# Kernel tuning notes

Measured on AMD Instinct MI355X. Metric: run time of the kernel, lower is better.

The kernel has to match this reference:

```python
import jax, jax.numpy as jnp
import numpy as np


def setup_inputs() -> dict:
    key = jax.random.key(0)
    ks = jax.random.split(key, 4)
    B, S, D, E = 8, 4096, 2048, 64
    scale = 1.0 / np.sqrt(D)
    return {
        "x": jax.random.normal(ks[0], (B, S, D), dtype=jnp.float32),
        "W_route": jax.random.normal(ks[1], (E, D), dtype=jnp.float32) * scale,
        "b_route": jnp.zeros((E,), dtype=jnp.float32),
        "W_noise": jax.random.normal(ks[2], (E, D), dtype=jnp.float32) * scale,
        "b_noise": jnp.zeros((E,), dtype=jnp.float32),
        "noise_eps": jax.random.normal(ks[3], (B, S, E), dtype=jnp.float32),
    }


TOP_K = 2


def reference(x, W_route, b_route, W_noise, b_noise, noise_eps):
    # Dual linear projections: [B,S,D] @ [D,E] -> [B,S,E]
    logits = jnp.einsum("bsd,ed->bse", x, W_route) + b_route
    noise_logits = jnp.einsum("bsd,ed->bse", x, W_noise) + b_noise
    noisy_logits = logits + noise_eps * jax.nn.softplus(noise_logits)

    B, S, E = noisy_logits.shape
    flat = noisy_logits.reshape(B * S, E)
    top_vals, top_idx = jax.lax.top_k(flat, TOP_K)  # [N,K]

    # Scatter top-k values into -inf background, then softmax over experts.
    neg_inf = jnp.full_like(flat, -jnp.inf)
    rows = jnp.arange(B * S)[:, None]
    sparse = neg_inf.at[rows, top_idx].set(top_vals)
    router_output = jax.nn.softmax(sparse, axis=-1).reshape(B, S, E)
    indices = top_idx.reshape(B, S, TOP_K)
    return router_output, indices
```

## Files before the change

kernel.cpp:

```cpp
#include <hip/hip_runtime.h>
#include <math.h>

typedef _Float16 f16;
typedef __attribute__((ext_vector_type(8))) _Float16 half8;
typedef __attribute__((ext_vector_type(4))) float f32x4;

#define NEXP 64
#define TM 64
#define L_STRIDE 132

__device__ __forceinline__ float softplus_f(float x) {
    return fmaxf(x, 0.0f) + log1pf(expf(-fabsf(x)));
}

__device__ __forceinline__ void lds_dma16(const void* g, void* l) {
    __builtin_amdgcn_global_load_lds(
        (const __attribute__((address_space(1))) unsigned int*)g,
        (__attribute__((address_space(3))) unsigned int*)l, 16, 0, 0);
}

__device__ __forceinline__ void cvt_split(const float4 a, const float4 b,
                                          half8& hv, half8& lv) {
    const float vv[8] = {a.x, a.y, a.z, a.w, b.x, b.y, b.z, b.w};
#pragma unroll
    for (int j = 0; j < 8; ++j) {
        const f16 h = (f16)vv[j];
        hv[j] = h;
        lv[j] = (f16)((vv[j] - (float)h) * 4096.0f);
    }
}

__global__ void wsplit_kernel(const float* __restrict__ Wr,
                              const float* __restrict__ Wn,
                              f16* __restrict__ ws, int D) {
    const int per_col = D >> 3;
    const int t = blockIdx.x * blockDim.x + threadIdx.x;
    const int col = t / per_col;
    const int k0  = (t - col * per_col) * 8;
    if (col >= 128) return;
    const float* src = (col < NEXP) ? &Wr[(size_t)col * D] : &Wn[(size_t)(col - NEXP) * D];
    const float4 v0 = *(const float4*)&src[k0];
    const float4 v1 = *(const float4*)&src[k0 + 4];
    half8 hi, lo;
    cvt_split(v0, v1, hi, lo);
    const int kc = k0 >> 5, q = (k0 >> 3) & 3;
    const size_t base = (size_t)kc * 8192 + (size_t)q * 1024 + (size_t)col * 8;
    *(half8*)&ws[base]        = hi;
    *(half8*)&ws[base + 4096] = lo;
}

__global__ __launch_bounds__(256, 3)
void router_mfma_kernel(const float* __restrict__ x,
                        const f16* __restrict__ wsW,
                        const float* __restrict__ br,
                        const float* __restrict__ bn,
                        const float* __restrict__ eps,
                        float* __restrict__ out,
                        int N, int D) {
    __shared__ union alignas(16) {
        struct { f16 B[2][8192]; f16 A[2][4096]; } st;
        float L[TM][L_STRIDE];
    } sm;
    __shared__ float biasLDS[128];
    __shared__ float p1s[TM], p2s[TM];
    __shared__ int   i1s[TM], i2s[TM];

    const int tid  = threadIdx.x;
    const int lane = tid & 63;
    const int w    = tid >> 6;
    const int rowbase = blockIdx.x * TM;
    const int wr = w & 1, wc = w >> 1;
    const int quad = lane >> 4;
    const int l16  = lane & 15;

    if (tid < 128) biasLDS[tid] = (tid < NEXP) ? br[tid] : bn[tid - NEXP];

    f32x4 accM[2][4], accC[2][4];
#pragma unroll
    for (int i = 0; i < 2; ++i)
#pragma unroll
        for (int j = 0; j < 4; ++j) {
            accM[i][j] = (f32x4){0.f, 0.f, 0.f, 0.f};
            accC[i][j] = (f32x4){0.f, 0.f, 0.f, 0.f};
        }

    const int sr = tid >> 2;
    const int sq = tid & 3;
    const float* xrow = &x[(size_t)(rowbase + sr) * D + sq * 8];
    const int nkc = D >> 5;

    {
        const char* gsrc = (const char*)wsW + (size_t)0 * 16384 + w * 4096 + lane * 16;
        char* ldst = (char*)&sm.st.B[0][0] + w * 4096;
#pragma unroll
        for (int i = 0; i < 4; ++i) lds_dma16(gsrc + i * 1024, ldst + i * 1024);
        const float4 a0 = *(const float4*)&xrow[0];
        const float4 a1 = *(const float4*)&xrow[4];
        half8 hv, lv;
        cvt_split(a0, a1, hv, lv);
        *(half8*)&sm.st.A[0][sq * 512 + sr * 8]        = hv;
        *(half8*)&sm.st.A[0][2048 + sq * 512 + sr * 8] = lv;
    }
    float4 v0 = *(const float4*)&xrow[32];
    float4 v1 = *(const float4*)&xrow[36];
    __syncthreads();

#pragma unroll 2
    for (int kc = 0; kc < nkc; ++kc) {
        const int cur = kc & 1, nxt = cur ^ 1;

        if (kc + 1 < nkc) {
            const char* gsrc = (const char*)wsW + (size_t)(kc + 1) * 16384 + w * 4096 + lane * 16;
            char* ldst = (char*)&sm.st.B[nxt][0] + w * 4096;
#pragma unroll
            for (int i = 0; i < 4; ++i) lds_dma16(gsrc + i * 1024, ldst + i * 1024);
            half8 hv, lv;
            cvt_split(v0, v1, hv, lv);
            *(half8*)&sm.st.A[nxt][sq * 512 + sr * 8]        = hv;
            *(half8*)&sm.st.A[nxt][2048 + sq * 512 + sr * 8] = lv;
        }
        if (kc + 2 < nkc) {
            v0 = *(const float4*)&xrow[(kc + 2) * 32];
            v1 = *(const float4*)&xrow[(kc + 2) * 32 + 4];
        }

        half8 ah[2], al[2], bh[4], bl[4];
#pragma unroll
        for (int rt = 0; rt < 2; ++rt) {
            const int r = (wr * 32 + rt * 16 + l16) * 8;
            ah[rt] = *(const half8*)&sm.st.A[cur][quad * 512 + r];
            al[rt] = *(const half8*)&sm.st.A[cur][2048 + quad * 512 + r];
        }
#pragma unroll
        for (int ct = 0; ct < 4; ++ct) {
            const int c = (wc * 64 + ct * 16 + l16) * 8;
            bh[ct] = *(const half8*)&sm.st.B[cur][quad * 1024 + c];
            bl[ct] = *(const half8*)&sm.st.B[cur][4096 + quad * 1024 + c];
        }

#pragma unroll
        for (int rt = 0; rt < 2; ++rt)
#pragma unroll
            for (int ct = 0; ct < 4; ++ct) {
                accM[rt][ct] = __builtin_amdgcn_mfma_f32_16x16x32_f16(ah[rt], bh[ct], accM[rt][ct], 0, 0, 0);
                accC[rt][ct] = __builtin_amdgcn_mfma_f32_16x16x32_f16(al[rt], bh[ct], accC[rt][ct], 0, 0, 0);
                accC[rt][ct] = __builtin_amdgcn_mfma_f32_16x16x32_f16(ah[rt], bl[ct], accC[rt][ct], 0, 0, 0);
            }
        __syncthreads();
    }

#pragma unroll
    for (int rt = 0; rt < 2; ++rt)
#pragma unroll
        for (int ct = 0; ct < 4; ++ct) {
            const int row = wr * 32 + rt * 16 + quad * 4;
            const int col = wc * 64 + ct * 16 + l16;
            const float bcol = biasLDS[col];
#pragma unroll
            for (int rg = 0; rg < 4; ++rg)
                sm.L[row + rg][col] = accM[rt][ct][rg] + accC[rt][ct][rg] * (1.0f / 4096.0f) + bcol;
        }
    __syncthreads();

#pragma unroll
    for (int t = 0; t < 4; ++t) {
        const int f   = tid * 4 + t * 1024;
        const int row = f >> 6;
        const int e0  = f & 63;
        const float4 ev = *(const float4*)&eps[(size_t)(rowbase + row) * NEXP + e0];
        const float evs[4] = {ev.x, ev.y, ev.z, ev.w};
#pragma unroll
        for (int j = 0; j < 4; ++j) {
            const float lg = sm.L[row][e0 + j];
            const float nz = sm.L[row][NEXP + e0 + j];
            sm.L[row][e0 + j] = fmaf(evs[j], softplus_f(nz), lg);
        }
    }
    __syncthreads();

    if (tid < TM) {
        const int r = tid;
        float v1t = -INFINITY, v2t = -INFINITY;
        int i1 = 0, i2 = 0;
#pragma unroll 8
        for (int e = 0; e < NEXP; ++e) {
            const float v = sm.L[r][e];
            if (v > v1t) { v2t = v1t; i2 = i1; v1t = v; i1 = e; }
            else if (v > v2t) { v2t = v; i2 = e; }
        }
        const float z = expf(v2t - v1t);
        const float s = 1.0f + z;
        p1s[r] = 1.0f / s;
        p2s[r] = z / s;
        i1s[r] = i1;
        i2s[r] = i2;
        float* oidx = out + (size_t)N * NEXP + (size_t)(rowbase + r) * 2;
        oidx[0] = (float)i1;
        oidx[1] = (float)i2;
    }
    __syncthreads();

    {
        const int r = tid >> 2;
        const int g = tid & 3;
        const float pa = p1s[r], pb = p2s[r];
        const int i1 = i1s[r], i2 = i2s[r];
        float* orow = out + (size_t)(rowbase + r) * NEXP;
#pragma unroll
        for (int t = 0; t < 4; ++t) {
            const int e0 = g * 16 + t * 4;
            float4 o;
            o.x = (e0 + 0 == i1) ? pa : ((e0 + 0 == i2) ? pb : 0.0f);
            o.y = (e0 + 1 == i1) ? pa : ((e0 + 1 == i2) ? pb : 0.0f);
            o.z = (e0 + 2 == i1) ? pa : ((e0 + 2 == i2) ? pb : 0.0f);
            o.w = (e0 + 3 == i1) ? pa : ((e0 + 3 == i2) ? pb : 0.0f);
            *(float4*)&orow[e0] = o;
        }
    }
}

#define BK 32
#define XS_STRIDE (TM + 4)
#define WS_STRIDE (128 + 4)

__global__ __launch_bounds__(256, 2)
void noisy_topk_router_kernel(const float* __restrict__ x,
                              const float* __restrict__ Wr,
                              const float* __restrict__ br,
                              const float* __restrict__ Wn,
                              const float* __restrict__ bn,
                              const float* __restrict__ eps,
                              float* __restrict__ out,
                              int N, int D) {
    __shared__ union alignas(16) {
        struct {
            float Xs[BK][XS_STRIDE];
            float Ws[BK][WS_STRIDE];
        } st;
        float L[TM][L_STRIDE];
    } sm;
    __shared__ float p1s[TM], p2s[TM];
    __shared__ int   i1s[TM], i2s[TM];

    const int tid = threadIdx.x;
    const int rowbase = blockIdx.x * TM;
    const int r0 = (tid >> 5) * 8;
    const int c0 = (tid & 31) * 4;

    float acc[8][4];
#pragma unroll
    for (int i = 0; i < 8; ++i)
#pragma unroll
        for (int j = 0; j < 4; ++j) acc[i][j] = 0.0f;

    const int q  = tid & 7;
    const int rr = tid >> 3;

    for (int k0 = 0; k0 < D; k0 += BK) {
#pragma unroll
        for (int i = 0; i < 2; ++i) {
            const int row = rr + 32 * i;
            const float4 xv = *(const float4*)&x[(size_t)(rowbase + row) * D + k0 + q * 4];
            sm.st.Xs[q * 4 + 0][row] = xv.x;
            sm.st.Xs[q * 4 + 1][row] = xv.y;
            sm.st.Xs[q * 4 + 2][row] = xv.z;
            sm.st.Xs[q * 4 + 3][row] = xv.w;
            const float4 wv = *(const float4*)&Wr[(size_t)row * D + k0 + q * 4];
            sm.st.Ws[q * 4 + 0][row] = wv.x;
            sm.st.Ws[q * 4 + 1][row] = wv.y;
            sm.st.Ws[q * 4 + 2][row] = wv.z;
            sm.st.Ws[q * 4 + 3][row] = wv.w;
            const float4 nv = *(const float4*)&Wn[(size_t)row * D + k0 + q * 4];
            sm.st.Ws[q * 4 + 0][NEXP + row] = nv.x;
            sm.st.Ws[q * 4 + 1][NEXP + row] = nv.y;
            sm.st.Ws[q * 4 + 2][NEXP + row] = nv.z;
            sm.st.Ws[q * 4 + 3][NEXP + row] = nv.w;
        }
        __syncthreads();
#pragma unroll 4
        for (int kk = 0; kk < BK; ++kk) {
            const float4 xa = *(const float4*)&sm.st.Xs[kk][r0];
            const float4 xb = *(const float4*)&sm.st.Xs[kk][r0 + 4];
            const float4 wv = *(const float4*)&sm.st.Ws[kk][c0];
            const float xs[8] = {xa.x, xa.y, xa.z, xa.w, xb.x, xb.y, xb.z, xb.w};
            const float ws[4] = {wv.x, wv.y, wv.z, wv.w};
#pragma unroll
            for (int i = 0; i < 8; ++i)
#pragma unroll
                for (int j = 0; j < 4; ++j)
                    acc[i][j] = fmaf(xs[i], ws[j], acc[i][j]);
        }
        __syncthreads();
    }
    {
        const float4 bv = (c0 < NEXP) ? *(const float4*)&br[c0]
                                      : *(const float4*)&bn[c0 - NEXP];
#pragma unroll
        for (int i = 0; i < 8; ++i) {
            float4 o;
            o.x = acc[i][0] + bv.x;
            o.y = acc[i][1] + bv.y;
            o.z = acc[i][2] + bv.z;
            o.w = acc[i][3] + bv.w;
            *(float4*)&sm.L[r0 + i][c0] = o;
        }
    }
    __syncthreads();
#pragma unroll
    for (int t = 0; t < 4; ++t) {
        const int f   = tid * 4 + t * 1024;
        const int row = f >> 6;
        const int e0  = f & 63;
        const float4 ev = *(const float4*)&eps[(size_t)(rowbase + row) * NEXP + e0];
        const float evs[4] = {ev.x, ev.y, ev.z, ev.w};
#pragma unroll
        for (int j = 0; j < 4; ++j) {
            const float lg = sm.L[row][e0 + j];
            const float nz = sm.L[row][NEXP + e0 + j];
            sm.L[row][e0 + j] = fmaf(evs[j], softplus_f(nz), lg);
        }
    }
    __syncthreads();
    if (tid < TM) {
        const int r = tid;
        float v1 = -INFINITY, v2 = -INFINITY;
        int i1 = 0, i2 = 0;
#pragma unroll 8
        for (int e = 0; e < NEXP; ++e) {
            const float v = sm.L[r][e];
            if (v > v1) { v2 = v1; i2 = i1; v1 = v; i1 = e; }
            else if (v > v2) { v2 = v; i2 = e; }
        }
        const float z = expf(v2 - v1);
        const float s = 1.0f + z;
        p1s[r] = 1.0f / s;
        p2s[r] = z / s;
        i1s[r] = i1;
        i2s[r] = i2;
        float* oidx = out + (size_t)N * NEXP + (size_t)(rowbase + r) * 2;
        oidx[0] = (float)i1;
        oidx[1] = (float)i2;
    }
    __syncthreads();
    {
        const int r = tid >> 2;
        const int g = tid & 3;
        const float pa = p1s[r], pb = p2s[r];
        const int i1 = i1s[r], i2 = i2s[r];
        float* orow = out + (size_t)(rowbase + r) * NEXP;
#pragma unroll
        for (int t = 0; t < 4; ++t) {
            const int e0 = g * 16 + t * 4;
            float4 o;
            o.x = (e0 + 0 == i1) ? pa : ((e0 + 0 == i2) ? pb : 0.0f);
            o.y = (e0 + 1 == i1) ? pa : ((e0 + 1 == i2) ? pb : 0.0f);
            o.z = (e0 + 2 == i1) ? pa : ((e0 + 2 == i2) ? pb : 0.0f);
            o.w = (e0 + 3 == i1) ? pa : ((e0 + 3 == i2) ? pb : 0.0f);
            *(float4*)&orow[e0] = o;
        }
    }
}

extern "C" void kernel_launch(void* const* d_in, const int* in_sizes, int n_in,
                              void* d_out, int out_size, void* d_ws, size_t ws_size,
                              hipStream_t stream) {
    const float* x   = (const float*)d_in[0];
    const float* Wr  = (const float*)d_in[1];
    const float* br  = (const float*)d_in[2];
    const float* Wn  = (const float*)d_in[3];
    const float* bn  = (const float*)d_in[4];
    const float* eps = (const float*)d_in[5];
    float* out = (float*)d_out;

    const int E = in_sizes[2];
    const int D = in_sizes[1] / E;
    const int N = in_sizes[0] / D;

    const size_t ws_needed = (size_t)128 * D * 2 * sizeof(f16);
    const bool fast = (E == 64) && (D == 2048) && (N % TM == 0) && (ws_size >= ws_needed);

    if (fast) {
        const int pre_threads = 128 * (D / 8);
        wsplit_kernel<<<(pre_threads + 255) / 256, 256, 0, stream>>>(Wr, Wn, (f16*)d_ws, D);
        router_mfma_kernel<<<N / TM, 256, 0, stream>>>(x, (const f16*)d_ws, br, bn, eps, out, N, D);
    } else {
        noisy_topk_router_kernel<<<N / TM, 256, 0, stream>>>(x, Wr, br, Wn, bn, eps, out, N, D);
    }
}
```

Measured before the change: 428.6 us.

## Deepen x prefetch to two stages with manual waitcnt and barriers

The fp32 x loads are now prefetched two K-chunks ahead using two register sets, and the loop is manually unrolled by two. The generic __syncthreads is replaced with explicit s_waitcnt vmcnt/lgkmcnt plus s_barrier, and sched_barriers pin the order of DMA issue, conversion and MFMA. The goal is to keep more global loads in flight so HBM latency is hidden behind the MFMA work. In exchange there are more live registers, and the vmcnt counts are hand-tuned, so correctness depends on the exact number of outstanding loads.

```diff
diff --git a/kernel.cpp b/kernel.cpp
--- a/kernel.cpp
+++ b/kernel.cpp
@@ -89,65 +89,92 @@
     const float* xrow = &x[(size_t)(rowbase + sr) * D + sq * 8];
     const int nkc = D >> 5;
 
+    float4 xva0, xva1, xvb0, xvb1;
+
     {
-        const char* gsrc = (const char*)wsW + (size_t)0 * 16384 + w * 4096 + lane * 16;
+        const char* gsrc = (const char*)wsW + w * 4096 + lane * 16;
         char* ldst = (char*)&sm.st.B[0][0] + w * 4096;
 #pragma unroll
         for (int i = 0; i < 4; ++i) lds_dma16(gsrc + i * 1024, ldst + i * 1024);
-        const float4 a0 = *(const float4*)&xrow[0];
-        const float4 a1 = *(const float4*)&xrow[4];
+        __builtin_amdgcn_sched_barrier(0);
+        const float4 c0a = *(const float4*)&xrow[0];
+        const float4 c0b = *(const float4*)&xrow[4];
+        __builtin_amdgcn_sched_barrier(0);
+        xva0 = *(const float4*)&xrow[32];
+        xva1 = *(const float4*)&xrow[36];
+        xvb0 = *(const float4*)&xrow[64];
+        xvb1 = *(const float4*)&xrow[68];
+        __builtin_amdgcn_sched_barrier(0);
         half8 hv, lv;
-        cvt_split(a0, a1, hv, lv);
+        cvt_split(c0a, c0b, hv, lv);
         *(half8*)&sm.st.A[0][sq * 512 + sr * 8]        = hv;
         *(half8*)&sm.st.A[0][2048 + sq * 512 + sr * 8] = lv;
-    }
-    float4 v0 = *(const float4*)&xrow[32];
-    float4 v1 = *(const float4*)&xrow[36];
-    __syncthreads();
-
-#pragma unroll 2
-    for (int kc = 0; kc < nkc; ++kc) {
-        const int cur = kc & 1, nxt = cur ^ 1;
-
-        if (kc + 1 < nkc) {
-            const char* gsrc = (const char*)wsW + (size_t)(kc + 1) * 16384 + w * 4096 + lane * 16;
-            char* ldst = (char*)&sm.st.B[nxt][0] + w * 4096;
-#pragma unroll
-            for (int i = 0; i < 4; ++i) lds_dma16(gsrc + i * 1024, ldst + i * 1024);
-            half8 hv, lv;
-            cvt_split(v0, v1, hv, lv);
-            *(half8*)&sm.st.A[nxt][sq * 512 + sr * 8]        = hv;
-            *(half8*)&sm.st.A[nxt][2048 + sq * 512 + sr * 8] = lv;
-        }
-        if (kc + 2 < nkc) {
-            v0 = *(const float4*)&xrow[(kc + 2) * 32];
-            v1 = *(const float4*)&xrow[(kc + 2) * 32 + 4];
-        }
-
-        half8 ah[2], al[2], bh[4], bl[4];
-#pragma unroll
-        for (int rt = 0; rt < 2; ++rt) {
-            const int r = (wr * 32 + rt * 16 + l16) * 8;
-            ah[rt] = *(const half8*)&sm.st.A[cur][quad * 512 + r];
-            al[rt] = *(const half8*)&sm.st.A[cur][2048 + quad * 512 + r];
-        }
-#pragma unroll
-        for (int ct = 0; ct < 4; ++ct) {
-            const int c = (wc * 64 + ct * 16 + l16) * 8;
-            bh[ct] = *(const half8*)&sm.st.B[cur][quad * 1024 + c];
-            bl[ct] = *(const half8*)&sm.st.B[cur][4096 + quad * 1024 + c];
-        }
-
-#pragma unroll
-        for (int rt = 0; rt < 2; ++rt)
-#pragma unroll
-            for (int ct = 0; ct < 4; ++ct) {
-                accM[rt][ct] = __builtin_amdgcn_mfma_f32_16x16x32_f16(ah[rt], bh[ct], accM[rt][ct], 0, 0, 0);
-                accC[rt][ct] = __builtin_amdgcn_mfma_f32_16x16x32_f16(al[rt], bh[ct], accC[rt][ct], 0, 0, 0);
-                accC[rt][ct] = __builtin_amdgcn_mfma_f32_16x16x32_f16(ah[rt], bl[ct], accC[rt][ct], 0, 0, 0);
-            }
-        __syncthreads();
-    }
+        asm volatile("s_waitcnt vmcnt(4) lgkmcnt(0)" : : : "memory");
+        __builtin_amdgcn_s_barrier();
+        __builtin_amdgcn_sched_barrier(0);
+    }
+
+#define KLOOP_BODY(KC, XV0, XV1)                                               \
+    {                                                                          \
+        const int cur = (KC) & 1, nxt = cur ^ 1;                               \
+        if ((KC) + 1 < nkc) {                                                  \
+            const char* gsrc = (const char*)wsW + (size_t)((KC) + 1) * 16384   \
+                               + w * 4096 + lane * 16;                         \
+            char* ldst = (char*)&sm.st.B[nxt][0] + w * 4096;                   \
+            lds_dma16(gsrc,        ldst);                                      \
+            lds_dma16(gsrc + 1024, ldst + 1024);                               \
+            lds_dma16(gsrc + 2048, ldst + 2048);                               \
+            lds_dma16(gsrc + 3072, ldst + 3072);                               \
+        }                                                                      \
+        __builtin_amdgcn_sched_barrier(0);                                     \
+        if ((KC) + 1 < nkc) {                                                  \
+            half8 hv, lv;                                                      \
+            cvt_split(XV0, XV1, hv, lv);                                       \
+            *(half8*)&sm.st.A[nxt][sq * 512 + sr * 8]        = hv;             \
+            *(half8*)&sm.st.A[nxt][2048 + sq * 512 + sr * 8] = lv;             \
+        }                                                                      \
+        if ((KC) + 3 < nkc) {                                                  \
+            XV0 = *(const float4*)&xrow[((KC) + 3) * 32];                      \
+            XV1 = *(const float4*)&xrow[((KC) + 3) * 32 + 4];                  \
+        }                                                                      \
+        __builtin_amdgcn_sched_barrier(0);                                     \
+        half8 ah[2], al[2], bh[4], bl[4];                                      \
+        _Pragma("unroll")                                                      \
+        for (int rt = 0; rt < 2; ++rt) {                                       \
+            const int r = (wr * 32 + rt * 16 + l16) * 8;                       \
+            ah[rt] = *(const half8*)&sm.st.A[cur][quad * 512 + r];             \
+            al[rt] = *(const half8*)&sm.st.A[cur][2048 + quad * 512 + r];      \
+        }                                                                      \
+        _Pragma("unroll")                                                      \
+        for (int ct = 0; ct < 4; ++ct) {                                       \
+            const int c = (wc * 64 + ct * 16 + l16) * 8;                       \
+            bh[ct] = *(const half8*)&sm.st.B[cur][quad * 1024 + c];            \
+            bl[ct] = *(const half8*)&sm.st.B[cur][4096 + quad * 1024 + c];     \
+        }                                                                      \
+        _Pragma("unroll")                                                      \
+        for (int rt = 0; rt < 2; ++rt)                                         \
+            _Pragma("unroll")                                                  \
+            for (int ct = 0; ct < 4; ++ct) {                                   \
+                accM[rt][ct] = __builtin_amdgcn_mfma_f32_16x16x32_f16(         \
+                    ah[rt], bh[ct], accM[rt][ct], 0, 0, 0);                    \
+                accC[rt][ct] = __builtin_amdgcn_mfma_f32_16x16x32_f16(         \
+                    al[rt], bh[ct], accC[rt][ct], 0, 0, 0);                    \
+                accC[rt][ct] = __builtin_amdgcn_mfma_f32_16x16x32_f16(         \
+                    ah[rt], bl[ct], accC[rt][ct], 0, 0, 0);                    \
+            }                                                                  \
+        if ((KC) + 3 < nkc)                                                    \
+            asm volatile("s_waitcnt vmcnt(2) lgkmcnt(0)" : : : "memory");      \
+        else                                                                   \
+            asm volatile("s_waitcnt vmcnt(0) lgkmcnt(0)" : : : "memory");      \
+        __builtin_amdgcn_s_barrier();                                          \
+        __builtin_amdgcn_sched_barrier(0);                                     \
+    }
+
+    for (int kc = 0; kc < nkc; kc += 2) {
+        KLOOP_BODY(kc,     xva0, xva1)
+        KLOOP_BODY(kc + 1, xvb0, xvb1)
+    }
+#undef KLOOP_BODY
 
 #pragma unroll
     for (int rt = 0; rt < 2; ++rt)
```

Measured after the change: 429.9 us. No clear change (+0.3%).
